# Kernel optimization log

Measured on AMD Instinct MI355X. Metric: run time of the kernel, lower is better.

## Reference

```python
import jax, jax.numpy as jnp
import numpy as np

# YOLOLayer config (matches init_kwargs)
ANCHORS = [(0.1, 0.13), (0.3, 0.35), (0.6, 0.55)]  # (w, h) as fraction of image
NUM_CLASSES = 80
STRIDE = 8
NA = len(ANCHORS)


def setup_inputs() -> dict:
    key = jax.random.key(0)
    B, C, G = 16, NA * (NUM_CLASSES + 5), 64
    x = jax.random.normal(key, (B, C, G, G), dtype=jnp.float32)
    return {"x": x}


def reference(x):
    B = x.shape[0]
    g0, g1 = x.shape[2], x.shape[3]
    nC = NUM_CLASSES
    # [B, nA, g0, g1, 5+nC]
    pred = x.reshape(B, NA, nC + 5, g0, g1).transpose(0, 1, 3, 4, 2)
    sx = jax.nn.sigmoid(pred[..., 0])
    sy = jax.nn.sigmoid(pred[..., 1])
    w = pred[..., 2]
    h = pred[..., 3]
    pred_conf = jax.nn.sigmoid(pred[..., 4])
    pred_cls = jax.nn.sigmoid(pred[..., 5:])

    # grid offsets: grid_x varies along last dim, grid_y along dim -2 (torch semantics)
    grid_x = jnp.arange(g1, dtype=x.dtype)[None, None, None, :]
    grid_y = jnp.arange(g0, dtype=x.dtype)[None, None, :, None]
    scaled = jnp.asarray([(aw * g0, ah * g1) for aw, ah in ANCHORS], dtype=x.dtype)
    anchor_w = scaled[:, 0].reshape(1, NA, 1, 1)
    anchor_h = scaled[:, 1].reshape(1, NA, 1, 1)

    # torch uses .data (detached) for pred_boxes -> stop_gradient for faithfulness
    pred_boxes = jnp.stack(
        [sx + grid_x, sy + grid_y, jnp.exp(w) * anchor_w, jnp.exp(h) * anchor_h],
        axis=-1,
    )
    pred_boxes = jax.lax.stop_gradient(pred_boxes)

    boxes = pred_boxes.reshape(B, -1, 4) * STRIDE
    conf = pred_conf.reshape(B, -1, 1)
    cls = pred_cls.reshape(B, -1, nC)
    return boxes, conf, cls
```

## Files before the change

kernel.cpp:

```cpp
#include <hip/hip_runtime.h>


#define NB 16
#define NA 3
#define NC 80
#define GG 4096
#define CH 85
#define S  64
#define NG (CH * (S / 4))
#define GPW (NG / 4)

typedef float f32x4 __attribute__((ext_vector_type(4)));

__device__ __forceinline__ float sigmoidf(float v) {
    return 1.0f / (1.0f + __expf(-v));
}

__device__ __forceinline__ int lidx(int ch, int p) {
    int g = (p >> 2) ^ ((ch >> 2) & 7);
    return (ch << 6) + (g << 2) + (p & 3);
}

__global__ __launch_bounds__(256) void yolo_kernel(const float* __restrict__ x,
                                                   float* __restrict__ out) {
    __shared__ float lds[2][CH * S];

    const int tid  = threadIdx.x;
    const int lane = tid & 63;
    const int wv   = tid >> 6;

    const int wg  = (blockIdx.x & 7) * 96 + (blockIdx.x >> 3);
    const int tg0 = wg * 4;

    float* __restrict__ boxesF = out;
    float* __restrict__ conf   = out + (size_t)NB * NA * GG * 4;
    f32x4* __restrict__ cls4   = (f32x4*)(out + (size_t)NB * NA * GG * 5);

    auto stage = [&](int tg, int buf) {
        const float* __restrict__ xin =
            x + (size_t)(tg >> 6) * CH * GG + (tg & 63) * S;
        #pragma unroll
        for (int it = 0; it < 6; ++it) {
            int g0 = wv * GPW + it * 64;
            if (it * 64 + lane < GPW) {
                int g   = g0 + lane;
                int ch  = g >> 4;
                int p4  = g & 15;
                int sp4 = p4 ^ ((ch >> 2) & 7);
                const float* gp = xin + (size_t)ch * GG + (sp4 << 2);
                float* lp = &lds[buf][g0 << 2];
                __builtin_amdgcn_global_load_lds(
                    (const __attribute__((address_space(1))) void*)gp,
                    (__attribute__((address_space(3))) void*)lp,
                    16, 0, 0);
            }
        }
    };

    auto compute = [&](int tg, int buf) {
        const float* __restrict__ L = lds[buf];
        const int ba  = tg >> 6;
        const int a   = ba % NA;
        const int row = tg & 63;
        const int loc = ba * GG + row * S;

        const float aw = (a == 0) ? 0.1f * 64 * 8
                       : (a == 1) ? 0.3f * 64 * 8 : 0.6f * 64 * 8;
        const float ah = (a == 0) ? 0.13f * 64 * 8
                       : (a == 1) ? 0.35f * 64 * 8 : 0.55f * 64 * 8;

        {
            int p    = wv * 16 + (lane >> 2);
            int comp = lane & 3;
            float v  = L[lidx(comp, p)];
            float e  = __expf(comp >= 2 ? v : -v);
            float sg = 1.0f / (1.0f + e);
            float gxy  = (comp == 0) ? (float)p : (float)row;
            float anch = (comp == 2) ? aw : ah;
            float r = (comp < 2) ? (sg + gxy) * 8.0f : e * anch;
            __builtin_nontemporal_store(
                r, &boxesF[((size_t)loc + wv * 16) * 4 + lane]);
            if (lane < 16) {
                float cv = sigmoidf(L[lidx(4, wv * 16 + lane)]);
                __builtin_nontemporal_store(cv, &conf[loc + wv * 16 + lane]);
            }
        }

        #pragma unroll
        for (int i0 = 0; i0 < 5; ++i0) {
            int i  = i0 * 256 + tid;
            int p  = i / 20;
            int c4 = i - p * 20;
            int r0 = 5 + (c4 << 2);
            f32x4 v;
            v.x = sigmoidf(L[lidx(r0 + 0, p)]);
            v.y = sigmoidf(L[lidx(r0 + 1, p)]);
            v.z = sigmoidf(L[lidx(r0 + 2, p)]);
            v.w = sigmoidf(L[lidx(r0 + 3, p)]);
            __builtin_nontemporal_store(v, &cls4[(size_t)loc * 20 + i]);
        }
    };

    stage(tg0 + 0, 0);
    stage(tg0 + 1, 1);
    asm volatile("s_waitcnt vmcnt(6)" ::: "memory");
    __builtin_amdgcn_s_barrier();
    __builtin_amdgcn_sched_barrier(0);
    compute(tg0 + 0, 0);
    __builtin_amdgcn_s_barrier();

    stage(tg0 + 2, 0);
    asm volatile("s_waitcnt vmcnt(13)" ::: "memory");
    __builtin_amdgcn_s_barrier();
    __builtin_amdgcn_sched_barrier(0);
    compute(tg0 + 1, 1);
    __builtin_amdgcn_s_barrier();

    stage(tg0 + 3, 1);
    asm volatile("s_waitcnt vmcnt(13)" ::: "memory");
    __builtin_amdgcn_s_barrier();
    __builtin_amdgcn_sched_barrier(0);
    compute(tg0 + 2, 0);

    asm volatile("s_waitcnt vmcnt(7)" ::: "memory");
    __builtin_amdgcn_s_barrier();
    __builtin_amdgcn_sched_barrier(0);
    compute(tg0 + 3, 1);
}

extern "C" void kernel_launch(void* const* d_in, const int* in_sizes, int n_in,
                              void* d_out, int out_size, void* d_ws, size_t ws_size,
                              hipStream_t stream) {
    const float* x = (const float*)d_in[0];
    float* out = (float*)d_out;
    yolo_kernel<<<dim3(768), 256, 0, stream>>>(x, out);
}
```

Measured before the change: 25.18 us.

## Use 512-thread blocks with 128-position tiles and single-buffered LDS staging

Doubles the tile to 128 spatial positions and the block to 512 threads, with each block handling two tiles instead of four. The double-buffered LDS pipeline with partial vmcnt waits is replaced by a single buffer: stage, wait for all loads, compute, then restage. This makes each block wider and the control flow simpler, but load and compute no longer overlap within a block, so latency hiding depends on other blocks resident on the same CU.

```diff
diff --git a/kernel.cpp b/kernel.cpp
--- a/kernel.cpp
+++ b/kernel.cpp
@@ -6,9 +6,9 @@
 #define NC 80
 #define GG 4096
 #define CH 85
-#define S  64
+#define S  128
 #define NG (CH * (S / 4))
-#define GPW (NG / 4)
+#define GPW (NG / 8)
 
 typedef float f32x4 __attribute__((ext_vector_type(4)));
 
@@ -18,37 +18,37 @@
 
 __device__ __forceinline__ int lidx(int ch, int p) {
     int g = (p >> 2) ^ ((ch >> 2) & 7);
-    return (ch << 6) + (g << 2) + (p & 3);
+    return (ch << 7) + (g << 2) + (p & 3);
 }
 
-__global__ __launch_bounds__(256) void yolo_kernel(const float* __restrict__ x,
+__global__ __launch_bounds__(512) void yolo_kernel(const float* __restrict__ x,
                                                    float* __restrict__ out) {
-    __shared__ float lds[2][CH * S];
+    __shared__ float lds[CH * S];
 
     const int tid  = threadIdx.x;
     const int lane = tid & 63;
     const int wv   = tid >> 6;
 
     const int wg  = (blockIdx.x & 7) * 96 + (blockIdx.x >> 3);
-    const int tg0 = wg * 4;
+    const int tg0 = wg * 2;
 
     float* __restrict__ boxesF = out;
     float* __restrict__ conf   = out + (size_t)NB * NA * GG * 4;
     f32x4* __restrict__ cls4   = (f32x4*)(out + (size_t)NB * NA * GG * 5);
 
-    auto stage = [&](int tg, int buf) {
+    auto stage = [&](int tg) {
         const float* __restrict__ xin =
-            x + (size_t)(tg >> 6) * CH * GG + (tg & 63) * S;
+            x + (size_t)(tg >> 5) * CH * GG + (tg & 31) * S;
         #pragma unroll
         for (int it = 0; it < 6; ++it) {
             int g0 = wv * GPW + it * 64;
             if (it * 64 + lane < GPW) {
                 int g   = g0 + lane;
-                int ch  = g >> 4;
-                int p4  = g & 15;
+                int ch  = g >> 5;
+                int p4  = g & 31;
                 int sp4 = p4 ^ ((ch >> 2) & 7);
                 const float* gp = xin + (size_t)ch * GG + (sp4 << 2);
-                float* lp = &lds[buf][g0 << 2];
+                float* lp = &lds[g0 << 2];
                 __builtin_amdgcn_global_load_lds(
                     (const __attribute__((address_space(1))) void*)gp,
                     (__attribute__((address_space(3))) void*)lp,
@@ -57,12 +57,13 @@
         }
     };
 
-    auto compute = [&](int tg, int buf) {
-        const float* __restrict__ L = lds[buf];
-        const int ba  = tg >> 6;
-        const int a   = ba % NA;
-        const int row = tg & 63;
-        const int loc = ba * GG + row * S;
+    auto compute = [&](int tg) {
+        const float* __restrict__ L = lds;
+        const int ba   = tg >> 5;
+        const int a    = ba % NA;
+        const int tpos = tg & 31;
+        const int s0   = tpos * S;
+        const int loc  = ba * GG + s0;
 
         const float aw = (a == 0) ? 0.1f * 64 * 8
                        : (a == 1) ? 0.3f * 64 * 8 : 0.6f * 64 * 8;
@@ -70,25 +71,25 @@
                        : (a == 1) ? 0.35f * 64 * 8 : 0.55f * 64 * 8;
 
         {
-            int p    = wv * 16 + (lane >> 2);
-            int comp = lane & 3;
+            int p    = tid >> 2;
+            int comp = tid & 3;
             float v  = L[lidx(comp, p)];
             float e  = __expf(comp >= 2 ? v : -v);
             float sg = 1.0f / (1.0f + e);
-            float gxy  = (comp == 0) ? (float)p : (float)row;
+            float gxy  = (comp == 0) ? (float)(p & 63)
+                                     : (float)((s0 + p) >> 6);
             float anch = (comp == 2) ? aw : ah;
             float r = (comp < 2) ? (sg + gxy) * 8.0f : e * anch;
             __builtin_nontemporal_store(
-                r, &boxesF[((size_t)loc + wv * 16) * 4 + lane]);
-            if (lane < 16) {
-                float cv = sigmoidf(L[lidx(4, wv * 16 + lane)]);
-                __builtin_nontemporal_store(cv, &conf[loc + wv * 16 + lane]);
-            }
+                r, &boxesF[(size_t)(loc + p) * 4 + comp]);
         }
+        if (tid < S)
+            __builtin_nontemporal_store(sigmoidf(L[lidx(4, tid)]),
+                                        &conf[loc + tid]);
 
         #pragma unroll
-        for (int i0 = 0; i0 < 5; ++i0) {
-            int i  = i0 * 256 + tid;
+        for (int it = 0; it < 5; ++it) {
+            int i  = it * 512 + tid;
             int p  = i / 20;
             int c4 = i - p * 20;
             int r0 = 5 + (c4 << 2);
@@ -101,31 +102,18 @@
         }
     };
 
-    stage(tg0 + 0, 0);
-    stage(tg0 + 1, 1);
-    asm volatile("s_waitcnt vmcnt(6)" ::: "memory");
+    stage(tg0);
+    asm volatile("s_waitcnt vmcnt(0)" ::: "memory");
     __builtin_amdgcn_s_barrier();
     __builtin_amdgcn_sched_barrier(0);
-    compute(tg0 + 0, 0);
+    compute(tg0);
+
     __builtin_amdgcn_s_barrier();
-
-    stage(tg0 + 2, 0);
-    asm volatile("s_waitcnt vmcnt(13)" ::: "memory");
+    stage(tg0 + 1);
+    asm volatile("s_waitcnt vmcnt(0)" ::: "memory");
     __builtin_amdgcn_s_barrier();
     __builtin_amdgcn_sched_barrier(0);
-    compute(tg0 + 1, 1);
-    __builtin_amdgcn_s_barrier();
-
-    stage(tg0 + 3, 1);
-    asm volatile("s_waitcnt vmcnt(13)" ::: "memory");
-    __builtin_amdgcn_s_barrier();
-    __builtin_amdgcn_sched_barrier(0);
-    compute(tg0 + 2, 0);
-
-    asm volatile("s_waitcnt vmcnt(7)" ::: "memory");
-    __builtin_amdgcn_s_barrier();
-    __builtin_amdgcn_sched_barrier(0);
-    compute(tg0 + 3, 1);
+    compute(tg0 + 1);
 }
 
 extern "C" void kernel_launch(void* const* d_in, const int* in_sizes, int n_in,
@@ -133,5 +121,5 @@
                               hipStream_t stream) {
     const float* x = (const float*)d_in[0];
     float* out = (float*)d_out;
-    yolo_kernel<<<dim3(768), 256, 0, stream>>>(x, out);
+    yolo_kernel<<<dim3(768), 512, 0, stream>>>(x, out);
 }
```

After: 25.11 us. Within noise of the previous version (-0.3%).
